# Kernel optimization log

Hardware: AMD Instinct MI355X
Metric: run time of the kernel (lower is better)

## Reference

```python
import jax, jax.numpy as jnp
import numpy as np

NUM_NODES = 1_200_000
NUM_FILLER = 200_000
NUM_PHYS = NUM_NODES - NUM_FILLER  # 1,000,000 physical nodes
NUM_MOVABLE = 900_000
NBX = NBY = 512
XL, XH, YL, YH = 0.0, 1000.0, 0.0, 1000.0
BSX = (XH - XL) / NBX
BSY = (YH - YL) / NBY
PIN_STRETCH = 1.4142135623730951
UNIT_PIN_CAP = 0.05
MAX_RATE = 1.5
MIN_RATE = 1.0 / MAX_RATE
K = 5  # max bins overlapped per dimension (span<=4.0, bin~1.95)


def _overlap_terms(lo, hi, bin_size, origin, nb):
    # lo, hi: [n] interval per node. Returns bin indices [n,K] and overlap lengths [n,K].
    il = jnp.clip(jnp.floor((lo - origin) / bin_size).astype(jnp.int32), 0, nb - 1)
    idx = il[:, None] + jnp.arange(K, dtype=jnp.int32)[None, :]
    valid = idx < nb
    idx = jnp.clip(idx, 0, nb - 1)
    b_lo = origin + idx.astype(lo.dtype) * bin_size
    ov = jnp.maximum(jnp.minimum(hi[:, None], b_lo + bin_size) - jnp.maximum(lo[:, None], b_lo), 0.0)
    return idx, jnp.where(valid, ov, 0.0)


def _forward(pos, node_size_x, node_size_y, flat_node2pin_start_map):
    P = NUM_PHYS
    sx, sy = node_size_x[:P], node_size_y[:P]
    # stretched half sizes: at least half a stretched bin
    hx = 0.5 * jnp.maximum(BSX * PIN_STRETCH, sx)
    hy = 0.5 * jnp.maximum(BSY * PIN_STRETCH, sy)
    cx = pos[:P] + 0.5 * sx
    cy = pos[NUM_NODES:NUM_NODES + P] + 0.5 * sy
    pw = (flat_node2pin_start_map[1:P + 1] - flat_node2pin_start_map[:P]).astype(pos.dtype)
    density = pw / (4.0 * hx * hy)  # pins per unit area over stretched bbox

    # stage 1: scatter stretched-bbox pin density into bin map
    ix, ovx = _overlap_terms(cx - hx, cx + hx, BSX, XL, NBX)  # [P,K]
    iy, ovy = _overlap_terms(cy - hy, cy + hy, BSY, YL, NBY)  # [P,K]
    contrib = ovx[:, :, None] * ovy[:, None, :] * density[:, None, None]  # [P,K,K]
    flat_idx = (ix[:, :, None] * NBY + iy[:, None, :]).reshape(-1)
    pin_map = jnp.zeros(NBX * NBY, dtype=pos.dtype).at[flat_idx].add(contrib.reshape(-1))

    # stage 2: pin utilization per bin, clamped adjust rate
    util = jnp.clip(pin_map / (BSX * BSY * UNIT_PIN_CAP), MIN_RATE, MAX_RATE)

    # stage 3: per movable node, integrate utilization over its (unstretched) bbox
    M = NUM_MOVABLE
    x_lo = pos[:M]
    x_hi = x_lo + node_size_x[:M]
    y_lo = pos[NUM_NODES:NUM_NODES + M]
    y_hi = y_lo + node_size_y[:M]
    jx, wx = _overlap_terms(x_lo, x_hi, BSX, XL, NBX)  # [M,K]
    jy, wy = _overlap_terms(y_lo, y_hi, BSY, YL, NBY)  # [M,K]
    u = util[jx[:, :, None] * NBY + jy[:, None, :]]  # [M,K,K]
    instance_pin_area = jnp.sum(wx[:, :, None] * wy[:, None, :] * u, axis=(1, 2))
    return instance_pin_area


def setup_inputs() -> dict:
    key = jax.random.key(0)
    k1, k2, k3, k4 = jax.random.split(key, 4)
    node_size_x = jax.random.uniform(k1, (NUM_NODES,), jnp.float32, 1.0, 4.0)
    node_size_y = jnp.full((NUM_NODES,), 2.0, jnp.float32)  # row height
    px = jax.random.uniform(k2, (NUM_NODES,), jnp.float32, 0.0, 995.0)
    py = jax.random.uniform(k3, (NUM_NODES,), jnp.float32, 0.0, 995.0)
    pos = jnp.concatenate([px, py])
    pin_counts = jax.random.randint(k4, (NUM_PHYS,), 1, 9, jnp.int32)
    flat = jnp.concatenate([jnp.zeros(1, jnp.int32), jnp.cumsum(pin_counts).astype(jnp.int32)])
    return {"pos": pos, "node_size_x": node_size_x, "node_size_y": node_size_y,
            "flat_node2pin_start_map": flat}


def reference(pos, node_size_x, node_size_y, flat_node2pin_start_map):
    return _forward(pos, node_size_x, node_size_y, flat_node2pin_start_map)
```

## Files before the change

### kernel.cpp

```cpp
#include <hip/hip_runtime.h>

#define NUM_NODES   1200000
#define NUM_FILLER  200000
#define NUM_PHYS    (NUM_NODES - NUM_FILLER)
#define NUM_MOVABLE 900000
#define NBX 512
#define NBY 512
#define NBINS (NBX * NBY)
#define BSX 1.953125f
#define BSY 1.953125f
#define PIN_STRETCH 1.4142135623730951f
#define CAP 0.19073486328125f
#define INV_CAP (1.0f / 0.19073486328125f)
#define MAX_RATE 1.5f
#define MIN_RATE (1.0f/1.5f)
#define K 5

#define TBITS   5
#define TSZ     32
#define TDIM    16
#define NTILES  (TDIM * TDIM)
#define HALO    (K - 1)
#define LTS     (TSZ + HALO)
#define SBLK    1024
#define NPB     4096
#define NBLK    ((NUM_PHYS + NPB - 1) / NPB)
#define MSTR    256

__device__ __forceinline__ int bin_lo(float lo) {
    int il = (int)floorf(lo / BSX);
    return min(max(il, 0), NBX - 1);
}

__device__ __forceinline__ float4 pack_rec(float cx, float cy, float hx, float hy, int pw) {
    unsigned pwm1 = (unsigned)(pw - 1) & 7u;
    unsigned ux = __float_as_uint(cx) | ((pwm1 & 1u) << 31);
    unsigned uy = __float_as_uint(cy) | (((pwm1 >> 1) & 1u) << 31);
    unsigned uz = __float_as_uint(hx) | (((pwm1 >> 2) & 1u) << 31);
    return make_float4(__uint_as_float(ux), __uint_as_float(uy),
                       __uint_as_float(uz), hy);
}

__global__ __launch_bounds__(SBLK) void sort_phys(
    const float* __restrict__ pos,
    const float* __restrict__ nsx,
    const float* __restrict__ nsy,
    const int*   __restrict__ flat,
    int*         __restrict__ cntArr,
    int*         __restrict__ offArr,
    float4*      __restrict__ rec,
    float*       __restrict__ pin)
{
    __shared__ int    cnt[NTILES];
    __shared__ int    pref[NTILES];
    __shared__ int    exc[NTILES];
    __shared__ int    lofs[NTILES];
    __shared__ float4 stage[NPB];
    int tid = threadIdx.x;
    int bid = blockIdx.x;
    if (tid < NTILES) cnt[tid] = 0;
    for (int i = bid * SBLK + tid; i < NBINS; i += NBLK * SBLK)
        pin[i] = 0.0f;
    __syncthreads();

    int q = bid * SBLK + tid;
    bool valid = (4 * q + 3) < NUM_PHYS;
    float4 r4[4];
    int tl[4] = {-1, -1, -1, -1};
    if (valid) {
        const float4* pos4  = (const float4*)pos;
        const float4* posy4 = (const float4*)(pos + NUM_NODES);
        const float4* nsx4  = (const float4*)nsx;
        const float4* nsy4  = (const float4*)nsy;
        float4 px = pos4[q], py = posy4[q];
        float4 sx = nsx4[q], sy = nsy4[q];
        int4 f4 = ((const int4*)flat)[q];
        int f5 = flat[4 * q + 4];
        float pxs[4] = {px.x, px.y, px.z, px.w};
        float pys[4] = {py.x, py.y, py.z, py.w};
        float sxs[4] = {sx.x, sx.y, sx.z, sx.w};
        float sys[4] = {sy.x, sy.y, sy.z, sy.w};
        int   pws[4] = {f4.y - f4.x, f4.z - f4.y, f4.w - f4.z, f5 - f4.w};
        #pragma unroll
        for (int j = 0; j < 4; ++j) {
            float hx = 0.5f * fmaxf(BSX * PIN_STRETCH, sxs[j]);
            float hy = 0.5f * fmaxf(BSY * PIN_STRETCH, sys[j]);
            float cx = pxs[j] + 0.5f * sxs[j];
            float cy = pys[j] + 0.5f * sys[j];
            r4[j] = pack_rec(cx, cy, hx, hy, pws[j]);
            int t = ((bin_lo(cx - hx) >> TBITS) << 4) | (bin_lo(cy - hy) >> TBITS);
            tl[j] = t;
            atomicAdd(&cnt[t], 1);
        }
    }
    __syncthreads();

    if (tid < NTILES) pref[tid] = cnt[tid];
    __syncthreads();
    #pragma unroll
    for (int off = 1; off < NTILES; off <<= 1) {
        int v = (tid < NTILES && tid >= off) ? pref[tid - off] : 0;
        __syncthreads();
        if (tid < NTILES) pref[tid] += v;
        __syncthreads();
    }
    if (tid < NTILES) {
        int e = pref[tid] - cnt[tid];
        exc[tid] = e;
        lofs[tid] = e;
        cntArr[tid * MSTR + bid] = cnt[tid];
        offArr[tid * MSTR + bid] = e;
    }
    __syncthreads();

    if (valid) {
        #pragma unroll
        for (int j = 0; j < 4; ++j) {
            int r = atomicAdd(&lofs[tl[j]], 1);
            stage[r] = r4[j];
        }
    }
    __syncthreads();

    int total = pref[NTILES - 1];
    float4* __restrict__ dst = rec + (size_t)bid * NPB;
    for (int k = tid; k < total; k += SBLK)
        dst[k] = stage[k];
}

__global__ __launch_bounds__(1024) void accumulate_tiles(
    const float4* __restrict__ rec,
    const int*    __restrict__ cntArr,
    const int*    __restrict__ offArr,
    float*        __restrict__ pin)
{
    __shared__ float tileA[LTS * LTS];
    __shared__ int cntB[NBLK];
    __shared__ int offB[NBLK];
    __shared__ int prefB[NBLK + 1];
    int tid = threadIdx.x;
    int t = blockIdx.x;
    int bx0 = (t >> 4) * TSZ, by0 = (t & 15) * TSZ;

    for (int i = tid; i < LTS * LTS; i += 1024) tileA[i] = 0.0f;
    if (tid < NBLK) {
        cntB[tid] = cntArr[t * MSTR + tid];
        offB[tid] = offArr[t * MSTR + tid];
    }
    __syncthreads();
    if (tid == 0) {
        int s = 0;
        for (int b = 0; b < NBLK; ++b) { prefB[b] = s; s += cntB[b]; }
        prefB[NBLK] = s;
    }
    __syncthreads();

    int total = prefB[NBLK];
    for (int k = tid; k < total; k += 1024) {
        int lo = 0, hi = NBLK;
        while (hi - lo > 1) {
            int mid = (lo + hi) >> 1;
            if (k >= prefB[mid]) lo = mid; else hi = mid;
        }
        float4 r = rec[(size_t)lo * NPB + offB[lo] + (k - prefB[lo])];
        unsigned ux = __float_as_uint(r.x), uy = __float_as_uint(r.y),
                 uz = __float_as_uint(r.z);
        float pw = (float)(1 + (int)((ux >> 31) | ((uy >> 31) << 1) | ((uz >> 31) << 2)));
        float cx = __uint_as_float(ux & 0x7fffffffu);
        float cy = __uint_as_float(uy & 0x7fffffffu);
        float hx = __uint_as_float(uz & 0x7fffffffu);
        float hy = r.w;
        float d = pw / (4.0f * hx * hy);
        float lox = cx - hx, hix = cx + hx;
        float loy = cy - hy, hiy = cy + hy;
        int il = bin_lo(lox), jl = bin_lo(loy);
        int ie = min(min((int)floorf(hix / BSX), NBX - 1), il + HALO);
        int je = min(min((int)floorf(hiy / BSY), NBY - 1), jl + HALO);
        int lr = il - bx0, lc = jl - by0;
        for (int a = il; a <= ie; ++a) {
            float blo = (float)a * BSX;
            float ox = fmaxf(fminf(hix, blo + BSX) - fmaxf(lox, blo), 0.0f);
            int rowb = (lr + (a - il)) * LTS + lc;
            for (int b2 = jl; b2 <= je; ++b2) {
                float blo2 = (float)b2 * BSY;
                float oy = fmaxf(fminf(hiy, blo2 + BSY) - fmaxf(loy, blo2), 0.0f);
                float cc = ox * oy * d;
                if (cc != 0.0f) atomicAdd(&tileA[rowb + (b2 - jl)], cc);
            }
        }
    }
    __syncthreads();
    for (int i = tid; i < LTS * LTS; i += 1024) {
        float v = tileA[i];
        int r = i / LTS, c = i % LTS;
        int gx = bx0 + r, gy = by0 + c;
        if (gx >= NBX || gy >= NBY) continue;
        bool interior = (r >= HALO) && (r < TSZ) && (c >= HALO) && (c < TSZ);
        if (interior) {
            if (v != 0.0f) pin[gx * NBY + gy] = v;
        } else {
            if (v != 0.0f) atomicAdd(&pin[gx * NBY + gy], v);
        }
    }
}

__global__ __launch_bounds__(256) void gather_pin_area(
    const float* __restrict__ pos,
    const float* __restrict__ nsx,
    const float* __restrict__ nsy,
    const float* __restrict__ pin,
    float*       __restrict__ out)
{
    int q = blockIdx.x * blockDim.x + threadIdx.x;
    if (q >= NUM_MOVABLE / 4) return;

    float4 xl4 = ((const float4*)pos)[q];
    float4 yl4 = ((const float4*)(pos + NUM_NODES))[q];
    float4 sx4 = ((const float4*)nsx)[q];
    float4 sy4 = ((const float4*)nsy)[q];

    float xls[4] = {xl4.x, xl4.y, xl4.z, xl4.w};
    float yls[4] = {yl4.x, yl4.y, yl4.z, yl4.w};
    float sxs[4] = {sx4.x, sx4.y, sx4.z, sx4.w};
    float sys[4] = {sy4.x, sy4.y, sy4.z, sy4.w};
    float res[4];

    #pragma unroll
    for (int j = 0; j < 4; ++j) {
        float xlo = xls[j], xhi = xlo + sxs[j];
        float ylo = yls[j], yhi = ylo + sys[j];
        int xb = min(bin_lo(xlo), NBX - 4);
        int yb = min(bin_lo(ylo), NBY - 3);

        float u[4][3];
        #pragma unroll
        for (int a = 0; a < 4; ++a) {
            const float* __restrict__ row = pin + (xb + a) * NBY + yb;
            u[a][0] = row[0]; u[a][1] = row[1]; u[a][2] = row[2];
        }
        float wx[4], wy[3];
        #pragma unroll
        for (int kx = 0; kx < 4; ++kx) {
            float blo = (float)(xb + kx) * BSX;
            wx[kx] = fmaxf(fminf(xhi, blo + BSX) - fmaxf(xlo, blo), 0.0f);
        }
        #pragma unroll
        for (int ky = 0; ky < 3; ++ky) {
            float blo = (float)(yb + ky) * BSY;
            wy[ky] = fmaxf(fminf(yhi, blo + BSY) - fmaxf(ylo, blo), 0.0f);
        }
        float acc = 0.0f;
        #pragma unroll
        for (int a = 0; a < 4; ++a)
            #pragma unroll
            for (int b = 0; b < 3; ++b) {
                float uc = fminf(fmaxf(u[a][b] * INV_CAP, MIN_RATE), MAX_RATE);
                acc += wx[a] * wy[b] * uc;
            }
        res[j] = acc;
    }
    ((float4*)out)[q] = make_float4(res[0], res[1], res[2], res[3]);
}

__global__ __launch_bounds__(256) void scatter_pin_map_agent(
    const float* __restrict__ pos,
    const float* __restrict__ nsx,
    const float* __restrict__ nsy,
    const int*   __restrict__ flat,
    float*       __restrict__ map)
{
    int p = blockIdx.x * blockDim.x + threadIdx.x;
    if (p >= NUM_PHYS) return;
    float sx = nsx[p], sy = nsy[p];
    float hx = 0.5f * fmaxf(BSX * PIN_STRETCH, sx);
    float hy = 0.5f * fmaxf(BSY * PIN_STRETCH, sy);
    float cx = pos[p] + 0.5f * sx;
    float cy = pos[NUM_NODES + p] + 0.5f * sy;
    float pw = (float)(flat[p + 1] - flat[p]);
    float density = pw / (4.0f * hx * hy);
    float lox = cx - hx, hixv = cx + hx;
    float loy = cy - hy, hiyv = cy + hy;
    int il = bin_lo(lox), jl = bin_lo(loy);
    int ie = min(min((int)floorf(hixv / BSX), NBX - 1), il + K - 1);
    int je = min(min((int)floorf(hiyv / BSY), NBY - 1), jl + K - 1);
    for (int a = il; a <= ie; ++a) {
        float blo = (float)a * BSX;
        float ox = fmaxf(fminf(hixv, blo + BSX) - fmaxf(lox, blo), 0.0f);
        for (int b = jl; b <= je; ++b) {
            float blo2 = (float)b * BSY;
            float oy = fmaxf(fminf(hiyv, blo2 + BSY) - fmaxf(loy, blo2), 0.0f);
            float c = ox * oy * density;
            if (c != 0.0f) atomicAdd(&map[a * NBY + b], c);
        }
    }
}

__global__ __launch_bounds__(256) void gather_general(
    const float* __restrict__ pos,
    const float* __restrict__ nsx,
    const float* __restrict__ nsy,
    const float* __restrict__ pin,
    float*       __restrict__ out)
{
    int m = blockIdx.x * blockDim.x + threadIdx.x;
    if (m >= NUM_MOVABLE) return;
    float xlo = pos[m];
    float xhi = xlo + nsx[m];
    float ylo = pos[NUM_NODES + m];
    float yhi = ylo + nsy[m];
    int il = bin_lo(xlo);
    int ie = min(min((int)floorf(xhi / BSX), NBX - 1), il + K - 1);
    int jl = bin_lo(ylo);
    int je = min(min((int)floorf(yhi / BSY), NBY - 1), jl + K - 1);
    float acc = 0.0f;
    for (int a = il; a <= ie; ++a) {
        float blo = (float)a * BSX;
        float wxv = fmaxf(fminf(xhi, blo + BSX) - fmaxf(xlo, blo), 0.0f);
        const float* __restrict__ row = pin + a * NBY;
        for (int b2 = jl; b2 <= je; ++b2) {
            float blo2 = (float)b2 * BSY;
            float wyv = fmaxf(fminf(yhi, blo2 + BSY) - fmaxf(ylo, blo2), 0.0f);
            float uc = fminf(fmaxf(row[b2] * INV_CAP, MIN_RATE), MAX_RATE);
            acc += wxv * wyv * uc;
        }
    }
    out[m] = acc;
}

extern "C" void kernel_launch(void* const* d_in, const int* in_sizes, int n_in,
                              void* d_out, int out_size, void* d_ws, size_t ws_size,
                              hipStream_t stream) {
    const float* pos  = (const float*)d_in[0];
    const float* nsx  = (const float*)d_in[1];
    const float* nsy  = (const float*)d_in[2];
    const int*   flat = (const int*)d_in[3];
    float* out = (float*)d_out;

    char* wsb = (char*)d_ws;
    float*  pin    = (float*)wsb;
    int*    cntArr = (int*)(wsb + (size_t)NBINS * 4);
    int*    offArr = cntArr + (size_t)NTILES * MSTR;
    float4* rec    = (float4*)(wsb + (size_t)NBINS * 4
                               + 2 * (size_t)NTILES * MSTR * 4);
    size_t needed = (size_t)NBINS * 4 + 2 * (size_t)NTILES * MSTR * 4
                  + (size_t)NBLK * NPB * 16;

    dim3 blk(256);
    if (ws_size >= needed) {
        sort_phys<<<NBLK, dim3(SBLK), 0, stream>>>(pos, nsx, nsy, flat,
                                                   cntArr, offArr, rec, pin);
        accumulate_tiles<<<NTILES, dim3(1024), 0, stream>>>(rec, cntArr, offArr, pin);
        gather_pin_area<<<(NUM_MOVABLE / 4 + 255) / 256, blk, 0, stream>>>(pos, nsx, nsy, pin, out);
    } else {
        hipMemsetAsync(pin, 0, (size_t)NBINS * 4, stream);
        scatter_pin_map_agent<<<(NUM_PHYS + 255) / 256, blk, 0, stream>>>(pos, nsx, nsy, flat, pin);
        gather_general<<<(NUM_MOVABLE + 255) / 256, blk, 0, stream>>>(pos, nsx, nsy, pin, out);
    }
}
```

Measured before the change: 138.6 us.

## Use 512 smaller tiles, halve per-thread node batches, parallelize block prefix scan

```diff
diff --git a/kernel.cpp b/kernel.cpp
--- a/kernel.cpp
+++ b/kernel.cpp
@@ -16,20 +16,24 @@
 #define MIN_RATE (1.0f/1.5f)
 #define K 5
 
-#define TBITS   5
-#define TSZ     32
-#define TDIM    16
-#define NTILES  (TDIM * TDIM)
+#define NT2     512
+#define TROW    16
+#define TCOL    32
 #define HALO    (K - 1)
-#define LTS     (TSZ + HALO)
+#define LROW    (TROW + HALO)
+#define LCOL    (TCOL + HALO)
 #define SBLK    1024
-#define NPB     4096
+#define NPB     2048
 #define NBLK    ((NUM_PHYS + NPB - 1) / NPB)
-#define MSTR    256
+#define MSTR    512
 
 __device__ __forceinline__ int bin_lo(float lo) {
     int il = (int)floorf(lo / BSX);
     return min(max(il, 0), NBX - 1);
+}
+
+__device__ __forceinline__ int tile_of(int il, int jl) {
+    return ((il >> 4) << 4) | (jl >> 5);
 }
 
 __device__ __forceinline__ float4 pack_rec(float cx, float cy, float hx, float hy, int pw) {
@@ -41,7 +45,7 @@
                        __uint_as_float(uz), hy);
 }
 
-__global__ __launch_bounds__(SBLK) void sort_phys(
+__global__ __launch_bounds__(SBLK, 8) void sort_phys(
     const float* __restrict__ pos,
     const float* __restrict__ nsx,
     const float* __restrict__ nsy,
@@ -51,62 +55,58 @@
     float4*      __restrict__ rec,
     float*       __restrict__ pin)
 {
-    __shared__ int    cnt[NTILES];
-    __shared__ int    pref[NTILES];
-    __shared__ int    exc[NTILES];
-    __shared__ int    lofs[NTILES];
+    __shared__ int    cnt[NT2];
+    __shared__ int    pref[NT2];
+    __shared__ int    lofs[NT2];
     __shared__ float4 stage[NPB];
     int tid = threadIdx.x;
     int bid = blockIdx.x;
-    if (tid < NTILES) cnt[tid] = 0;
+    if (tid < NT2) cnt[tid] = 0;
     for (int i = bid * SBLK + tid; i < NBINS; i += NBLK * SBLK)
         pin[i] = 0.0f;
     __syncthreads();
 
     int q = bid * SBLK + tid;
-    bool valid = (4 * q + 3) < NUM_PHYS;
-    float4 r4[4];
-    int tl[4] = {-1, -1, -1, -1};
+    bool valid = (2 * q + 1) < NUM_PHYS;
+    float4 r2[2];
+    int tl[2] = {-1, -1};
     if (valid) {
-        const float4* pos4  = (const float4*)pos;
-        const float4* posy4 = (const float4*)(pos + NUM_NODES);
-        const float4* nsx4  = (const float4*)nsx;
-        const float4* nsy4  = (const float4*)nsy;
-        float4 px = pos4[q], py = posy4[q];
-        float4 sx = nsx4[q], sy = nsy4[q];
-        int4 f4 = ((const int4*)flat)[q];
-        int f5 = flat[4 * q + 4];
-        float pxs[4] = {px.x, px.y, px.z, px.w};
-        float pys[4] = {py.x, py.y, py.z, py.w};
-        float sxs[4] = {sx.x, sx.y, sx.z, sx.w};
-        float sys[4] = {sy.x, sy.y, sy.z, sy.w};
-        int   pws[4] = {f4.y - f4.x, f4.z - f4.y, f4.w - f4.z, f5 - f4.w};
-        #pragma unroll
-        for (int j = 0; j < 4; ++j) {
+        float2 px = ((const float2*)pos)[q];
+        float2 py = ((const float2*)(pos + NUM_NODES))[q];
+        float2 sx = ((const float2*)nsx)[q];
+        float2 sy = ((const float2*)nsy)[q];
+        int2 f2 = ((const int2*)flat)[q];
+        int f3 = flat[2 * q + 2];
+        float pxs[2] = {px.x, px.y};
+        float pys[2] = {py.x, py.y};
+        float sxs[2] = {sx.x, sx.y};
+        float sys[2] = {sy.x, sy.y};
+        int   pws[2] = {f2.y - f2.x, f3 - f2.y};
+        #pragma unroll
+        for (int j = 0; j < 2; ++j) {
             float hx = 0.5f * fmaxf(BSX * PIN_STRETCH, sxs[j]);
             float hy = 0.5f * fmaxf(BSY * PIN_STRETCH, sys[j]);
             float cx = pxs[j] + 0.5f * sxs[j];
             float cy = pys[j] + 0.5f * sys[j];
-            r4[j] = pack_rec(cx, cy, hx, hy, pws[j]);
-            int t = ((bin_lo(cx - hx) >> TBITS) << 4) | (bin_lo(cy - hy) >> TBITS);
+            r2[j] = pack_rec(cx, cy, hx, hy, pws[j]);
+            int t = tile_of(bin_lo(cx - hx), bin_lo(cy - hy));
             tl[j] = t;
             atomicAdd(&cnt[t], 1);
         }
     }
     __syncthreads();
 
-    if (tid < NTILES) pref[tid] = cnt[tid];
+    if (tid < NT2) pref[tid] = cnt[tid];
     __syncthreads();
     #pragma unroll
-    for (int off = 1; off < NTILES; off <<= 1) {
-        int v = (tid < NTILES && tid >= off) ? pref[tid - off] : 0;
+    for (int off = 1; off < NT2; off <<= 1) {
+        int v = (tid < NT2 && tid >= off) ? pref[tid - off] : 0;
         __syncthreads();
-        if (tid < NTILES) pref[tid] += v;
+        if (tid < NT2) pref[tid] += v;
         __syncthreads();
     }
-    if (tid < NTILES) {
+    if (tid < NT2) {
         int e = pref[tid] - cnt[tid];
-        exc[tid] = e;
         lofs[tid] = e;
         cntArr[tid * MSTR + bid] = cnt[tid];
         offArr[tid * MSTR + bid] = e;
@@ -115,44 +115,51 @@
 
     if (valid) {
         #pragma unroll
-        for (int j = 0; j < 4; ++j) {
+        for (int j = 0; j < 2; ++j) {
             int r = atomicAdd(&lofs[tl[j]], 1);
-            stage[r] = r4[j];
-        }
-    }
-    __syncthreads();
-
-    int total = pref[NTILES - 1];
+            stage[r] = r2[j];
+        }
+    }
+    __syncthreads();
+
+    int total = pref[NT2 - 1];
     float4* __restrict__ dst = rec + (size_t)bid * NPB;
     for (int k = tid; k < total; k += SBLK)
         dst[k] = stage[k];
 }
 
-__global__ __launch_bounds__(1024) void accumulate_tiles(
+__global__ __launch_bounds__(1024, 8) void accumulate_tiles(
     const float4* __restrict__ rec,
     const int*    __restrict__ cntArr,
     const int*    __restrict__ offArr,
     float*        __restrict__ pin)
 {
-    __shared__ float tileA[LTS * LTS];
+    __shared__ float tileA[LROW * LCOL];
     __shared__ int cntB[NBLK];
     __shared__ int offB[NBLK];
     __shared__ int prefB[NBLK + 1];
+    __shared__ int sc[MSTR];
     int tid = threadIdx.x;
     int t = blockIdx.x;
-    int bx0 = (t >> 4) * TSZ, by0 = (t & 15) * TSZ;
-
-    for (int i = tid; i < LTS * LTS; i += 1024) tileA[i] = 0.0f;
+    int bx0 = (t >> 4) * TROW, by0 = (t & 15) * TCOL;
+
+    if (tid < LROW * LCOL) tileA[tid] = 0.0f;
     if (tid < NBLK) {
         cntB[tid] = cntArr[t * MSTR + tid];
         offB[tid] = offArr[t * MSTR + tid];
     }
     __syncthreads();
-    if (tid == 0) {
-        int s = 0;
-        for (int b = 0; b < NBLK; ++b) { prefB[b] = s; s += cntB[b]; }
-        prefB[NBLK] = s;
-    }
+    if (tid < MSTR) sc[tid] = (tid < NBLK) ? cntB[tid] : 0;
+    __syncthreads();
+    #pragma unroll
+    for (int off = 1; off < MSTR; off <<= 1) {
+        int v = (tid < MSTR && tid >= off) ? sc[tid - off] : 0;
+        __syncthreads();
+        if (tid < MSTR) sc[tid] += v;
+        __syncthreads();
+    }
+    if (tid < NBLK) prefB[tid] = sc[tid] - cntB[tid];
+    if (tid == MSTR - 1) prefB[NBLK] = sc[MSTR - 1];
     __syncthreads();
 
     int total = prefB[NBLK];
@@ -180,7 +187,7 @@
         for (int a = il; a <= ie; ++a) {
             float blo = (float)a * BSX;
             float ox = fmaxf(fminf(hix, blo + BSX) - fmaxf(lox, blo), 0.0f);
-            int rowb = (lr + (a - il)) * LTS + lc;
+            int rowb = (lr + (a - il)) * LCOL + lc;
             for (int b2 = jl; b2 <= je; ++b2) {
                 float blo2 = (float)b2 * BSY;
                 float oy = fmaxf(fminf(hiy, blo2 + BSY) - fmaxf(loy, blo2), 0.0f);
@@ -190,16 +197,17 @@
         }
     }
     __syncthreads();
-    for (int i = tid; i < LTS * LTS; i += 1024) {
-        float v = tileA[i];
-        int r = i / LTS, c = i % LTS;
+    if (tid < LROW * LCOL) {
+        float v = tileA[tid];
+        int r = tid / LCOL, c = tid % LCOL;
         int gx = bx0 + r, gy = by0 + c;
-        if (gx >= NBX || gy >= NBY) continue;
-        bool interior = (r >= HALO) && (r < TSZ) && (c >= HALO) && (c < TSZ);
-        if (interior) {
-            if (v != 0.0f) pin[gx * NBY + gy] = v;
-        } else {
-            if (v != 0.0f) atomicAdd(&pin[gx * NBY + gy], v);
+        if (gx < NBX && gy < NBY) {
+            bool interior = (r >= HALO) && (r < TROW) && (c >= HALO) && (c < TCOL);
+            if (interior) {
+                if (v != 0.0f) pin[gx * NBY + gy] = v;
+            } else {
+                if (v != 0.0f) atomicAdd(&pin[gx * NBY + gy], v);
+            }
         }
     }
 }
@@ -212,21 +220,21 @@
     float*       __restrict__ out)
 {
     int q = blockIdx.x * blockDim.x + threadIdx.x;
-    if (q >= NUM_MOVABLE / 4) return;
-
-    float4 xl4 = ((const float4*)pos)[q];
-    float4 yl4 = ((const float4*)(pos + NUM_NODES))[q];
-    float4 sx4 = ((const float4*)nsx)[q];
-    float4 sy4 = ((const float4*)nsy)[q];
-
-    float xls[4] = {xl4.x, xl4.y, xl4.z, xl4.w};
-    float yls[4] = {yl4.x, yl4.y, yl4.z, yl4.w};
-    float sxs[4] = {sx4.x, sx4.y, sx4.z, sx4.w};
-    float sys[4] = {sy4.x, sy4.y, sy4.z, sy4.w};
-    float res[4];
+    if (q >= NUM_MOVABLE / 2) return;
+
+    float2 xl2 = ((const float2*)pos)[q];
+    float2 yl2 = ((const float2*)(pos + NUM_NODES))[q];
+    float2 sx2 = ((const float2*)nsx)[q];
+    float2 sy2 = ((const float2*)nsy)[q];
+
+    float xls[2] = {xl2.x, xl2.y};
+    float yls[2] = {yl2.x, yl2.y};
+    float sxs[2] = {sx2.x, sx2.y};
+    float sys[2] = {sy2.x, sy2.y};
+    float res[2];
 
     #pragma unroll
-    for (int j = 0; j < 4; ++j) {
+    for (int j = 0; j < 2; ++j) {
         float xlo = xls[j], xhi = xlo + sxs[j];
         float ylo = yls[j], yhi = ylo + sys[j];
         int xb = min(bin_lo(xlo), NBX - 4);
@@ -259,7 +267,7 @@
             }
         res[j] = acc;
     }
-    ((float4*)out)[q] = make_float4(res[0], res[1], res[2], res[3]);
+    ((float2*)out)[q] = make_float2(res[0], res[1]);
 }
 
 __global__ __launch_bounds__(256) void scatter_pin_map_agent(
@@ -339,18 +347,18 @@
     char* wsb = (char*)d_ws;
     float*  pin    = (float*)wsb;
     int*    cntArr = (int*)(wsb + (size_t)NBINS * 4);
-    int*    offArr = cntArr + (size_t)NTILES * MSTR;
+    int*    offArr = cntArr + (size_t)NT2 * MSTR;
     float4* rec    = (float4*)(wsb + (size_t)NBINS * 4
-                               + 2 * (size_t)NTILES * MSTR * 4);
-    size_t needed = (size_t)NBINS * 4 + 2 * (size_t)NTILES * MSTR * 4
+                               + 2 * (size_t)NT2 * MSTR * 4);
+    size_t needed = (size_t)NBINS * 4 + 2 * (size_t)NT2 * MSTR * 4
                   + (size_t)NBLK * NPB * 16;
 
     dim3 blk(256);
     if (ws_size >= needed) {
         sort_phys<<<NBLK, dim3(SBLK), 0, stream>>>(pos, nsx, nsy, flat,
                                                    cntArr, offArr, rec, pin);
-        accumulate_tiles<<<NTILES, dim3(1024), 0, stream>>>(rec, cntArr, offArr, pin);
-        gather_pin_area<<<(NUM_MOVABLE / 4 + 255) / 256, blk, 0, stream>>>(pos, nsx, nsy, pin, out);
+        accumulate_tiles<<<NT2, dim3(1024), 0, stream>>>(rec, cntArr, offArr, pin);
+        gather_pin_area<<<(NUM_MOVABLE / 2 + 255) / 256, blk, 0, stream>>>(pos, nsx, nsy, pin, out);
     } else {
         hipMemsetAsync(pin, 0, (size_t)NBINS * 4, stream);
         scatter_pin_map_agent<<<(NUM_PHYS + 255) / 256, blk, 0, stream>>>(pos, nsx, nsy, flat, pin);
```

New measurement: 136.6 us (median of 2 runs). No clear change (-1.4%).
